# Kernel tuning notes

Hardware: AMD Instinct MI355X
Metric: run time of the kernel (lower is better)

Reference implementation:

```python
import jax, jax.numpy as jnp
import numpy as np

N_NODES, N_VARS, E = 100000, 50000, 640000
FEAT, H, L = 16, 128, 4
N_INT, K = 20000, 8  # integer vars with categorical heads, uniform domain size


def _mlp2(x, W1, b1, W2, b2):
    return jnp.maximum(x @ W1 + b1, 0.0) @ W2 + b2


def setup_inputs() -> dict:
    key = jax.random.key(0)
    ks = jax.random.split(key, 24)
    s = lambda i, shape, scale: jax.random.normal(ks[i], shape, dtype=jnp.float32) * scale
    inp = {
        "x": jax.random.normal(ks[0], (N_NODES, FEAT), dtype=jnp.float32),
        "edge_index": jax.random.randint(ks[1], (2, E), 0, N_NODES, dtype=jnp.int32).astype(jnp.int64),
        "num_vars": N_VARS,
        # NodeEmbedder (var / cons)
        "ve_W1": s(2, (FEAT, H), 0.25), "ve_b1": jnp.zeros((H,), jnp.float32),
        "ve_W2": s(3, (H, H), 0.09),   "ve_b2": jnp.zeros((H,), jnp.float32),
        "ce_W1": s(4, (FEAT, H), 0.25), "ce_b1": jnp.zeros((H,), jnp.float32),
        "ce_W2": s(5, (H, H), 0.09),   "ce_b2": jnp.zeros((H,), jnp.float32),
        # GCN backbone: stacked per-layer params
        "conv_W": s(6, (L, H, H), 0.09), "conv_b": jnp.zeros((L, H), jnp.float32),
        "ref_W1": s(7, (L, H, H), 0.09), "ref_b1": jnp.zeros((L, H), jnp.float32),
        "ref_W2": s(8, (L, H, H), 0.09), "ref_b2": jnp.zeros((L, H), jnp.float32),
        # Bernoulli head: H -> H//2 -> 1
        "bh_W1": s(9, (H, H // 2), 0.09), "bh_b1": jnp.zeros((H // 2,), jnp.float32),
        "bh_W2": s(10, (H // 2, 1), 0.12), "bh_b2": jnp.zeros((1,), jnp.float32),
        # Categorical heads: one Linear(H, K) per integer variable, batched
        "cat_W": s(11, (N_INT, H, K), 0.09),
        "cat_b": jnp.zeros((N_INT, K), jnp.float32),
    }
    return inp


def reference(x, edge_index, num_vars,
              ve_W1, ve_b1, ve_W2, ve_b2,
              ce_W1, ce_b1, ce_W2, ce_b2,
              conv_W, conv_b, ref_W1, ref_b1, ref_W2, ref_b2,
              bh_W1, bh_b1, bh_W2, bh_b2,
              cat_W, cat_b):
    N = x.shape[0]
    src, dst = edge_index[0], edge_index[1]
    # GCN normalization with self-loops: deg includes the self edge
    deg = jax.ops.segment_sum(jnp.ones((src.shape[0],), x.dtype), dst, num_segments=N) + 1.0
    dinv_sqrt = jax.lax.rsqrt(deg)
    enorm = dinv_sqrt[src] * dinv_sqrt[dst]      # [E]
    self_norm = (1.0 / deg)[:, None]             # [N,1] self-loop weight deg^-1

    var_h = _mlp2(x[:num_vars], ve_W1, ve_b1, ve_W2, ve_b2)
    cons_h = _mlp2(x[num_vars:], ce_W1, ce_b1, ce_W2, ce_b2)
    h = jnp.concatenate([var_h, cons_h], axis=0)  # [N,H]

    def gcn_conv(xin, W, b):
        hw = xin @ W
        agg = jax.ops.segment_sum(hw[src] * enorm[:, None], dst, num_segments=N)
        return agg + hw * self_norm + b

    def layer(xc, p):
        W, b, W1, b1, W2, b2 = p
        h_ = jnp.maximum(gcn_conv(xc, W, b), 0.0)
        return xc + _mlp2(h_, W1, b1, W2, b2), None

    h, _ = jax.lax.scan(layer, h, (conv_W, conv_b, ref_W1, ref_b1, ref_W2, ref_b2))

    vh = h[:num_vars]
    bern_logits = _mlp2(vh, bh_W1, bh_b1, bh_W2, bh_b2)[:, 0]          # [num_vars]
    n_int = cat_W.shape[0]
    cat_logits = jnp.einsum('nh,nhk->nk', vh[:n_int], cat_W) + cat_b    # [n_int,K]
    return bern_logits, cat_logits
```

## Files before the change

### kernel.cpp

```cpp
#include <hip/hip_runtime.h>
#include <hip/hip_bf16.h>

#define NN 100000
#define NV 50000
#define NE 640000
#define FEAT 16
#define HD 128
#define NL 4
#define NI 20000
#define KK 8
#define SCAN_BLK 98
#define LDP 136
#define WE_STRIDE (128*32 + 128*128)

typedef __hip_bfloat16 bf16;
typedef __attribute__((ext_vector_type(8))) short short8;
typedef __attribute__((ext_vector_type(4))) float f32x4;

static __device__ __forceinline__ ushort f2bu(float f) {
    __hip_bfloat16 b = __float2bfloat16(f);
    return *reinterpret_cast<ushort*>(&b);
}
static __device__ __forceinline__ float bu2f(ushort u) {
    __hip_bfloat16 b = *reinterpret_cast<__hip_bfloat16*>(&u);
    return __bfloat162float(b);
}

__global__ void k_deg_init(float* deg) {
    int i = blockIdx.x * blockDim.x + threadIdx.x;
    if (i < NN) deg[i] = 1.0f;
}

__global__ void k_deg_scatter(const int* __restrict__ ei, float* deg) {
    int e = blockIdx.x * blockDim.x + threadIdx.x;
    if (e < NE) atomicAdd(&deg[ei[NE + e]], 1.0f);
}

__global__ void k_deg_fin(const float* __restrict__ deg, float* dinv, float* selfn) {
    int i = blockIdx.x * blockDim.x + threadIdx.x;
    if (i < NN) {
        float d = deg[i];
        dinv[i]  = rsqrtf(d);
        selfn[i] = 1.0f / d;
    }
}

__global__ void k_scan_part(const float* __restrict__ deg, int* __restrict__ part) {
    __shared__ int s[256];
    const int t = threadIdx.x;
    const int i = blockIdx.x * 1024 + t * 4;
    int sum = 0;
#pragma unroll
    for (int j = 0; j < 4; ++j)
        if (i + j < NN) sum += (int)deg[i + j] - 1;
    s[t] = sum;
    __syncthreads();
    for (int off = 128; off > 0; off >>= 1) {
        if (t < off) s[t] += s[t + off];
        __syncthreads();
    }
    if (t == 0) part[blockIdx.x] = s[0];
}

__global__ void k_scan_mid(const int* __restrict__ part, int* __restrict__ blockoff,
                           int* __restrict__ row_ptr) {
    __shared__ int s[128];
    const int t = threadIdx.x;
    int v = (t < SCAN_BLK) ? part[t] : 0;
    s[t] = v;
    __syncthreads();
    for (int off = 1; off < 128; off <<= 1) {
        int u = (t >= off) ? s[t - off] : 0;
        __syncthreads();
        s[t] += u;
        __syncthreads();
    }
    if (t < SCAN_BLK) blockoff[t] = s[t] - v;
    if (t == 0) row_ptr[NN] = NE;
}

__global__ void k_scan_apply(const float* __restrict__ deg,
                             const int* __restrict__ blockoff,
                             int* __restrict__ row_ptr, int* __restrict__ cnt) {
    __shared__ int s[256];
    const int t = threadIdx.x;
    const int i = blockIdx.x * 1024 + t * 4;
    int c[4];
    int tsum = 0;
#pragma unroll
    for (int j = 0; j < 4; ++j) {
        c[j] = (i + j < NN) ? (int)deg[i + j] - 1 : 0;
        tsum += c[j];
    }
    s[t] = tsum;
    __syncthreads();
    for (int off = 1; off < 256; off <<= 1) {
        int u = (t >= off) ? s[t - off] : 0;
        __syncthreads();
        s[t] += u;
        __syncthreads();
    }
    int off = blockoff[blockIdx.x] + s[t] - tsum;
#pragma unroll
    for (int j = 0; j < 4; ++j) {
        if (i + j < NN) {
            row_ptr[i + j] = off;
            cnt[i + j] = 0;
            off += c[j];
        }
    }
}

__global__ void k_csr_fill(const int* __restrict__ ei,
                           const int* __restrict__ row_ptr, int* __restrict__ cnt,
                           const float* __restrict__ dinv,
                           int* __restrict__ col, float* __restrict__ wgt) {
    int e = blockIdx.x * blockDim.x + threadIdx.x;
    if (e >= NE) return;
    const int s = ei[e];
    const int d = ei[NE + e];
    const int pos = row_ptr[d] + atomicAdd(&cnt[d], 1);
    col[pos] = s;
    wgt[pos] = dinv[s] * dinv[d];
}

__global__ void k_wprep(const float* __restrict__ conv_W,
                        const float* __restrict__ ref_W1,
                        const float* __restrict__ ref_W2,
                        ushort* __restrict__ wt) {
    const int mat = blockIdx.x >> 7;
    const int j = blockIdx.x & 127;
    const int k = threadIdx.x;
    const float* src = (mat < 4) ? conv_W + (size_t)mat * HD * HD
                     : (mat < 8) ? ref_W1 + (size_t)(mat - 4) * HD * HD
                                 : ref_W2 + (size_t)(mat - 8) * HD * HD;
    wt[(size_t)mat * HD * HD + j * HD + k] = f2bu(src[k * HD + j]);
}

__global__ void k_wprep_embed(const float* __restrict__ vW1, const float* __restrict__ vW2,
                              const float* __restrict__ cW1, const float* __restrict__ cW2,
                              ushort* __restrict__ wte) {
    const int side = blockIdx.x >> 7;
    const int j = blockIdx.x & 127;
    const int k = threadIdx.x;
    const float* W1 = side ? cW1 : vW1;
    const float* W2 = side ? cW2 : vW2;
    ushort* o = wte + (size_t)side * WE_STRIDE;
    if (k < 32) o[j * 32 + k] = (k < FEAT) ? f2bu(W1[k * HD + j]) : (ushort)0;
    o[128 * 32 + j * HD + k] = f2bu(W2[k * HD + j]);
}

__global__ __launch_bounds__(256, 4) void k_embed_mfma(
        const float* __restrict__ x,
        const ushort* __restrict__ W1t, const float* __restrict__ b1,
        const ushort* __restrict__ W2t, const float* __restrict__ b2,
        int nbase, int nend,
        ushort* __restrict__ hb) {
    const int lane = threadIdx.x & 63, w = threadIdx.x >> 6;
    const int l15 = lane & 15, lg = lane >> 4;
    const int rowb = nbase + blockIdx.x * 128;
    __shared__ ushort hsm[128][LDP];

#pragma unroll
    for (int rt = 0; rt < 2; ++rt) {
        const int r = rowb + w * 32 + rt * 16 + l15;
        const int rc = r < nend ? r : nend - 1;
        short8 a = {0, 0, 0, 0, 0, 0, 0, 0};
        if (lg < 2) {
            const float* xp = x + (size_t)rc * FEAT + lg * 8;
#pragma unroll
            for (int i = 0; i < 8; ++i) a[i] = (short)f2bu(xp[i]);
        }
#pragma unroll
        for (int jt = 0; jt < 8; ++jt) {
            const float bv = b1[jt * 16 + l15];
            f32x4 acc = {bv, bv, bv, bv};
            short8 b = *reinterpret_cast<const short8*>(&W1t[(jt * 16 + l15) * 32 + lg * 8]);
            acc = __builtin_amdgcn_mfma_f32_16x16x32_bf16(a, b, acc, 0, 0, 0);
#pragma unroll
            for (int rr = 0; rr < 4; ++rr)
                hsm[w * 32 + rt * 16 + lg * 4 + rr][jt * 16 + l15] =
                    f2bu(fmaxf(acc[rr], 0.0f));
        }
    }
    __syncthreads();

#pragma unroll
    for (int rt = 0; rt < 2; ++rt) {
        f32x4 acc[8];
#pragma unroll
        for (int jt = 0; jt < 8; ++jt) {
            const float bv = b2[jt * 16 + l15];
            f32x4 v = {bv, bv, bv, bv};
            acc[jt] = v;
        }
#pragma unroll
        for (int ks = 0; ks < 4; ++ks) {
            short8 a = *reinterpret_cast<const short8*>(&hsm[w * 32 + rt * 16 + l15][ks * 32 + lg * 8]);
#pragma unroll
            for (int jt = 0; jt < 8; ++jt) {
                short8 b = *reinterpret_cast<const short8*>(&W2t[(jt * 16 + l15) * HD + ks * 32 + lg * 8]);
                acc[jt] = __builtin_amdgcn_mfma_f32_16x16x32_bf16(a, b, acc[jt], 0, 0, 0);
            }
        }
#pragma unroll
        for (int jt = 0; jt < 8; ++jt)
#pragma unroll
            for (int rr = 0; rr < 4; ++rr) {
                const int row = rowb + w * 32 + rt * 16 + lg * 4 + rr;
                if (row < nend)
                    hb[(size_t)row * HD + jt * 16 + l15] = f2bu(acc[jt][rr]);
            }
    }
}

__global__ __launch_bounds__(256) void k_hw(
                     const ushort* __restrict__ hb, const ushort* __restrict__ Wt,
                     ushort* __restrict__ hwb) {
    const int lane = threadIdx.x & 63;
    const int w = threadIdx.x >> 6;
    const int row0 = blockIdx.x * 128 + w * 32;
    const int l15 = lane & 15, lg = lane >> 4;

    const f32x4 zero = {0.f, 0.f, 0.f, 0.f};
    f32x4 acc[2][8];
#pragma unroll
    for (int rt = 0; rt < 2; ++rt)
#pragma unroll
        for (int jt = 0; jt < 8; ++jt) acc[rt][jt] = zero;

#pragma unroll
    for (int ks = 0; ks < 4; ++ks) {
        short8 a[2];
#pragma unroll
        for (int rt = 0; rt < 2; ++rt) {
            int r = row0 + rt * 16 + l15;
            r = r < NN ? r : NN - 1;
            a[rt] = *reinterpret_cast<const short8*>(&hb[(size_t)r * HD + ks * 32 + lg * 8]);
        }
#pragma unroll
        for (int jt = 0; jt < 8; ++jt) {
            short8 b = *reinterpret_cast<const short8*>(&Wt[(jt * 16 + l15) * HD + ks * 32 + lg * 8]);
            acc[0][jt] = __builtin_amdgcn_mfma_f32_16x16x32_bf16(a[0], b, acc[0][jt], 0, 0, 0);
            acc[1][jt] = __builtin_amdgcn_mfma_f32_16x16x32_bf16(a[1], b, acc[1][jt], 0, 0, 0);
        }
    }
#pragma unroll
    for (int rt = 0; rt < 2; ++rt)
#pragma unroll
        for (int jt = 0; jt < 8; ++jt)
#pragma unroll
            for (int r = 0; r < 4; ++r) {
                int row = row0 + rt * 16 + lg * 4 + r;
                if (row < NN) hwb[(size_t)row * HD + jt * 16 + l15] = f2bu(acc[rt][jt][r]);
            }
}

__global__ __launch_bounds__(512, 4) void k_combine(
                          const ushort* __restrict__ hwb,
                          const int* __restrict__ row_ptr,
                          const int* __restrict__ col,
                          const float* __restrict__ wgt,
                          const float* __restrict__ selfn,
                          const float* __restrict__ cb,
                          const ushort* __restrict__ Wt1, const float* __restrict__ b1,
                          const ushort* __restrict__ Wt2, const float* __restrict__ b2,
                          ushort* __restrict__ hb) {
    const int t = threadIdx.x;
    const int n0 = blockIdx.x * 64;
    __shared__ ushort hs[64][LDP];
    __shared__ ushort hid[64][LDP];
    __shared__ int rp[65];

    if (t <= 64) {
        int idx = n0 + t;
        rp[t] = row_ptr[idx < NN ? idx : NN];
    }
    __syncthreads();

    const int lane = t & 63, w = t >> 6;
    {
        const int c0 = 2 * lane;
        const float cbx = cb[c0], cby = cb[c0 + 1];
        float accx[8], accy[8];
        int ecur[8], eend[8];
        int rounds = 0;
#pragma unroll
        for (int m = 0; m < 8; ++m) {
            const int node = n0 + w * 8 + m;
            const int nc = node < NN ? node : NN - 1;
            const uint hv = *reinterpret_cast<const uint*>(&hwb[(size_t)nc * HD + c0]);
            const float sn = selfn[nc];
            accx[m] = bu2f((ushort)(hv & 0xffffu)) * sn + cbx;
            accy[m] = bu2f((ushort)(hv >> 16)) * sn + cby;
            ecur[m] = rp[w * 8 + m];
            eend[m] = rp[w * 8 + m + 1];
            rounds = max(rounds, eend[m] - ecur[m]);
        }
#pragma unroll 1
        for (int r = 0; r < rounds; r += 2) {
            uint va[8], vb[8];
            float wa[8], wb[8];
            int ca[8], cc[8];
#pragma unroll
            for (int m = 0; m < 8; ++m) {
                const int e0 = ecur[m];
                const int a0 = (e0 < eend[m]) ? e0 : 0;
                const int a1 = (e0 + 1 < eend[m]) ? e0 + 1 : 0;
                wa[m] = (e0 < eend[m]) ? wgt[a0] : 0.0f;
                wb[m] = (e0 + 1 < eend[m]) ? wgt[a1] : 0.0f;
                ca[m] = col[a0];
                cc[m] = col[a1];
            }
#pragma unroll
            for (int m = 0; m < 8; ++m) {
                va[m] = *reinterpret_cast<const uint*>(&hwb[(size_t)ca[m] * HD + c0]);
                vb[m] = *reinterpret_cast<const uint*>(&hwb[(size_t)cc[m] * HD + c0]);
            }
#pragma unroll
            for (int m = 0; m < 8; ++m) {
                accx[m] += wa[m] * bu2f((ushort)(va[m] & 0xffffu));
                accy[m] += wa[m] * bu2f((ushort)(va[m] >> 16));
                accx[m] += wb[m] * bu2f((ushort)(vb[m] & 0xffffu));
                accy[m] += wb[m] * bu2f((ushort)(vb[m] >> 16));
            }
#pragma unroll
            for (int m = 0; m < 8; ++m) ecur[m] += 2;
        }
#pragma unroll
        for (int m = 0; m < 8; ++m) {
            const uint px = (uint)f2bu(fmaxf(accx[m], 0.0f));
            const uint py = (uint)f2bu(fmaxf(accy[m], 0.0f));
            *reinterpret_cast<uint*>(&hs[w * 8 + m][c0]) = px | (py << 16);
        }
    }
    __syncthreads();

    const int l15 = lane & 15, lg = lane >> 4;
    const int rt = (w & 3) * 16;
    const int c0 = (w >> 2) * 64;

    f32x4 acc1[4];
#pragma unroll
    for (int jt = 0; jt < 4; ++jt) {
        float bv = b1[c0 + jt * 16 + l15];
        f32x4 v = {bv, bv, bv, bv};
        acc1[jt] = v;
    }
#pragma unroll
    for (int ks = 0; ks < 4; ++ks) {
        short8 a = *reinterpret_cast<const short8*>(&hs[rt + l15][ks * 32 + lg * 8]);
#pragma unroll
        for (int jt = 0; jt < 4; ++jt) {
            short8 b = *reinterpret_cast<const short8*>(&Wt1[(c0 + jt * 16 + l15) * HD + ks * 32 + lg * 8]);
            acc1[jt] = __builtin_amdgcn_mfma_f32_16x16x32_bf16(a, b, acc1[jt], 0, 0, 0);
        }
    }
#pragma unroll
    for (int jt = 0; jt < 4; ++jt)
#pragma unroll
        for (int r = 0; r < 4; ++r)
            hid[rt + lg * 4 + r][c0 + jt * 16 + l15] = f2bu(fmaxf(acc1[jt][r], 0.0f));
    __syncthreads();

    f32x4 acc2[4];
#pragma unroll
    for (int jt = 0; jt < 4; ++jt) {
        float bv = b2[c0 + jt * 16 + l15];
        f32x4 v = {bv, bv, bv, bv};
        acc2[jt] = v;
    }
#pragma unroll
    for (int ks = 0; ks < 4; ++ks) {
        short8 a = *reinterpret_cast<const short8*>(&hid[rt + l15][ks * 32 + lg * 8]);
#pragma unroll
        for (int jt = 0; jt < 4; ++jt) {
            short8 b = *reinterpret_cast<const short8*>(&Wt2[(c0 + jt * 16 + l15) * HD + ks * 32 + lg * 8]);
            acc2[jt] = __builtin_amdgcn_mfma_f32_16x16x32_bf16(a, b, acc2[jt], 0, 0, 0);
        }
    }
#pragma unroll
    for (int jt = 0; jt < 4; ++jt)
#pragma unroll
        for (int r = 0; r < 4; ++r) {
            const int row = n0 + rt + lg * 4 + r;
            if (row < NN) {
                const size_t idx = (size_t)row * HD + c0 + jt * 16 + l15;
                hb[idx] = f2bu(acc2[jt][r] + bu2f(hb[idx]));
            }
        }
}

__global__ void k_bern(const ushort* __restrict__ hb,
                       const float* __restrict__ W1, const float* __restrict__ b1,
                       const float* __restrict__ W2, const float* __restrict__ b2,
                       float* __restrict__ out) {
    const long long t = (long long)blockIdx.x * blockDim.x + threadIdx.x;
    const int n = (int)(t >> 6);
    const int lane = (int)(t & 63);
    if (n >= NV) return;
    const ushort* hn = hb + (size_t)n * HD;
    float acc = b1[lane];
#pragma unroll 8
    for (int k = 0; k < HD; ++k) acc += bu2f(hn[k]) * W1[k * 64 + lane];
    float p = fmaxf(acc, 0.0f) * W2[lane];
#pragma unroll
    for (int off = 32; off > 0; off >>= 1) p += __shfl_down(p, off);
    if (lane == 0) out[n] = p + b2[0];
}

__global__ void k_cat(const ushort* __restrict__ hb,
                      const float* __restrict__ cW, const float* __restrict__ cb,
                      float* __restrict__ out) {
    const long long t = (long long)blockIdx.x * blockDim.x + threadIdx.x;
    const int n = (int)(t >> 6);
    const int lane = (int)(t & 63);
    if (n >= NI) return;
    const ushort* hn = hb + (size_t)n * HD;
    float p[KK];
#pragma unroll
    for (int k = 0; k < KK; ++k) p[k] = 0.0f;
#pragma unroll
    for (int half = 0; half < 2; ++half) {
        const int hh = lane + 64 * half;
        const float vh = bu2f(hn[hh]);
        const float* wp = cW + ((size_t)n * HD + hh) * KK;
#pragma unroll
        for (int k = 0; k < KK; ++k) p[k] += vh * wp[k];
    }
#pragma unroll
    for (int k = 0; k < KK; ++k) {
#pragma unroll
        for (int off = 32; off > 0; off >>= 1) p[k] += __shfl_down(p[k], off);
    }
    if (lane == 0) {
#pragma unroll
        for (int k = 0; k < KK; ++k) out[NV + (size_t)n * KK + k] = p[k] + cb[(size_t)n * KK + k];
    }
}

extern "C" void kernel_launch(void* const* d_in, const int* in_sizes, int n_in,
                              void* d_out, int out_size, void* d_ws, size_t ws_size,
                              hipStream_t stream) {
    const float* x  = (const float*)d_in[0];
    const int*   ei = (const int*)d_in[1];
    const float* ve_W1 = (const float*)d_in[3];
    const float* ve_b1 = (const float*)d_in[4];
    const float* ve_W2 = (const float*)d_in[5];
    const float* ve_b2 = (const float*)d_in[6];
    const float* ce_W1 = (const float*)d_in[7];
    const float* ce_b1 = (const float*)d_in[8];
    const float* ce_W2 = (const float*)d_in[9];
    const float* ce_b2 = (const float*)d_in[10];
    const float* conv_W = (const float*)d_in[11];
    const float* conv_b = (const float*)d_in[12];
    const float* ref_W1 = (const float*)d_in[13];
    const float* ref_b1 = (const float*)d_in[14];
    const float* ref_W2 = (const float*)d_in[15];
    const float* ref_b2 = (const float*)d_in[16];
    const float* bh_W1 = (const float*)d_in[17];
    const float* bh_b1 = (const float*)d_in[18];
    const float* bh_W2 = (const float*)d_in[19];
    const float* bh_b2 = (const float*)d_in[20];
    const float* cat_W = (const float*)d_in[21];
    const float* cat_b = (const float*)d_in[22];
    float* out = (float*)d_out;

    const size_t need = (size_t)(3 * NN + (NN + 1) + NN + 2 * NE + 2 * SCAN_BLK) * 4
                      + (size_t)NN * HD * 2
                      + (size_t)NN * HD * 2
                      + (size_t)12 * HD * HD * 2
                      + (size_t)2 * WE_STRIDE * 2;
    if (ws_size < need) return;

    float* deg     = (float*)d_ws;
    float* dinv    = deg + NN;
    float* selfn   = dinv + NN;
    int*   row_ptr = (int*)(selfn + NN);
    int*   cnt     = row_ptr + (NN + 1);
    int*   col     = cnt + NN;
    float* wgt     = (float*)(col + NE);
    int*   part    = (int*)(wgt + NE);
    int*   blockoff= part + SCAN_BLK;
    ushort* hwb    = (ushort*)(blockoff + SCAN_BLK);
    ushort* hb     = hwb + (size_t)NN * HD;
    ushort* wt     = hb + (size_t)NN * HD;
    ushort* wte    = wt + (size_t)12 * HD * HD;

    k_deg_init<<<(NN + 255) / 256, 256, 0, stream>>>(deg);
    k_deg_scatter<<<(NE + 255) / 256, 256, 0, stream>>>(ei, deg);
    k_deg_fin<<<(NN + 255) / 256, 256, 0, stream>>>(deg, dinv, selfn);
    k_scan_part<<<SCAN_BLK, 256, 0, stream>>>(deg, part);
    k_scan_mid<<<1, 128, 0, stream>>>(part, blockoff, row_ptr);
    k_scan_apply<<<SCAN_BLK, 256, 0, stream>>>(deg, blockoff, row_ptr, cnt);
    k_csr_fill<<<(NE + 255) / 256, 256, 0, stream>>>(ei, row_ptr, cnt, dinv, col, wgt);
    k_wprep<<<12 * 128, 128, 0, stream>>>(conv_W, ref_W1, ref_W2, wt);
    k_wprep_embed<<<256, 128, 0, stream>>>(ve_W1, ve_W2, ce_W1, ce_W2, wte);

    k_embed_mfma<<<(NV + 127) / 128, 256, 0, stream>>>(
        x, wte, ve_b1, wte + 128 * 32, ve_b2, 0, NV, hb);
    k_embed_mfma<<<(NN - NV + 127) / 128, 256, 0, stream>>>(
        x, wte + WE_STRIDE, ce_b1, wte + WE_STRIDE + 128 * 32, ce_b2, NV, NN, hb);

    for (int l = 0; l < NL; ++l) {
        k_hw<<<(NN + 127) / 128, 256, 0, stream>>>(hb, wt + (size_t)l * HD * HD, hwb);
        k_combine<<<(NN + 63) / 64, 512, 0, stream>>>(hwb, row_ptr, col, wgt, selfn,
                                               conv_b + (size_t)l * HD,
                                               wt + (size_t)(4 + l) * HD * HD,
                                               ref_b1 + (size_t)l * HD,
                                               wt + (size_t)(8 + l) * HD * HD,
                                               ref_b2 + (size_t)l * HD,
                                               hb);
    }

    k_bern<<<(NV * 64) / 256, 256, 0, stream>>>(hb, bh_W1, bh_b1, bh_W2, bh_b2, out);
    k_cat<<<(NI * 64) / 256, 256, 0, stream>>>(hb, cat_W, cat_b, out);
}
```

Measured before the change: 769.4 us.

## Fuse layer-0 hw matmul into embed, shrink combine blocks, vectorize cat loads

The embed kernel now also multiplies the freshly computed embedding by the first conv weight and writes hw for layer 0, so the separate k_hw launch for layer 0 is skipped along with one re-read of h. The combine kernel moves from 64 nodes and 512 threads per block to 32 nodes and 256 threads, with more blocks resident per CU. The categorical head loads its weights with float4 vector loads. The workspace also reserves an extra hw buffer (hwbB) that nothing uses.

After: 1.197 ms. 1.56x slower.

```diff
diff --git a/kernel.cpp b/kernel.cpp
--- a/kernel.cpp
+++ b/kernel.cpp
@@ -1,5 +1,6 @@
 #include <hip/hip_runtime.h>
 #include <hip/hip_bf16.h>
+
 
 #define NN 100000
 #define NV 50000
@@ -9,6 +10,7 @@
 #define NL 4
 #define NI 20000
 #define KK 8
+#define NB 32
 #define SCAN_BLK 98
 #define LDP 136
 #define WE_STRIDE (128*32 + 128*128)
@@ -154,8 +156,9 @@
         const float* __restrict__ x,
         const ushort* __restrict__ W1t, const float* __restrict__ b1,
         const ushort* __restrict__ W2t, const float* __restrict__ b2,
+        const ushort* __restrict__ Wtc,
         int nbase, int nend,
-        ushort* __restrict__ hb) {
+        ushort* __restrict__ hb, ushort* __restrict__ hwb) {
     const int lane = threadIdx.x & 63, w = threadIdx.x >> 6;
     const int l15 = lane & 15, lg = lane >> 4;
     const int rowb = nbase + blockIdx.x * 128;
@@ -208,8 +211,30 @@
 #pragma unroll
             for (int rr = 0; rr < 4; ++rr) {
                 const int row = rowb + w * 32 + rt * 16 + lg * 4 + rr;
+                const ushort hv = f2bu(acc[jt][rr]);
+                if (row < nend) hb[(size_t)row * HD + jt * 16 + l15] = hv;
+                hsm[w * 32 + rt * 16 + lg * 4 + rr][jt * 16 + l15] = hv;
+            }
+        f32x4 acc3[8];
+        const f32x4 zero = {0.f, 0.f, 0.f, 0.f};
+#pragma unroll
+        for (int jt = 0; jt < 8; ++jt) acc3[jt] = zero;
+#pragma unroll
+        for (int ks = 0; ks < 4; ++ks) {
+            short8 a = *reinterpret_cast<const short8*>(&hsm[w * 32 + rt * 16 + l15][ks * 32 + lg * 8]);
+#pragma unroll
+            for (int jt = 0; jt < 8; ++jt) {
+                short8 b = *reinterpret_cast<const short8*>(&Wtc[(jt * 16 + l15) * HD + ks * 32 + lg * 8]);
+                acc3[jt] = __builtin_amdgcn_mfma_f32_16x16x32_bf16(a, b, acc3[jt], 0, 0, 0);
+            }
+        }
+#pragma unroll
+        for (int jt = 0; jt < 8; ++jt)
+#pragma unroll
+            for (int rr = 0; rr < 4; ++rr) {
+                const int row = rowb + w * 32 + rt * 16 + lg * 4 + rr;
                 if (row < nend)
-                    hb[(size_t)row * HD + jt * 16 + l15] = f2bu(acc[jt][rr]);
+                    hwb[(size_t)row * HD + jt * 16 + l15] = f2bu(acc3[jt][rr]);
             }
     }
 }
@@ -256,7 +281,7 @@
             }
 }
 
-__global__ __launch_bounds__(512, 4) void k_combine(
+__global__ __launch_bounds__(256, 8) void k_combine(
                           const ushort* __restrict__ hwb,
                           const int* __restrict__ row_ptr,
                           const int* __restrict__ col,
@@ -267,12 +292,12 @@
                           const ushort* __restrict__ Wt2, const float* __restrict__ b2,
                           ushort* __restrict__ hb) {
     const int t = threadIdx.x;
-    const int n0 = blockIdx.x * 64;
-    __shared__ ushort hs[64][LDP];
-    __shared__ ushort hid[64][LDP];
-    __shared__ int rp[65];
-
-    if (t <= 64) {
+    const int n0 = blockIdx.x * NB;
+    __shared__ ushort hs[NB][LDP];
+    __shared__ ushort hid[NB][LDP];
+    __shared__ int rp[NB + 1];
+
+    if (t <= NB) {
         int idx = n0 + t;
         rp[t] = row_ptr[idx < NN ? idx : NN];
     }
@@ -337,8 +362,8 @@
     __syncthreads();
 
     const int l15 = lane & 15, lg = lane >> 4;
-    const int rt = (w & 3) * 16;
-    const int c0 = (w >> 2) * 64;
+    const int rt = (w & 1) * 16;
+    const int c0 = (w >> 1) * 64;
 
     f32x4 acc1[4];
 #pragma unroll
@@ -425,8 +450,10 @@
         const int hh = lane + 64 * half;
         const float vh = bu2f(hn[hh]);
         const float* wp = cW + ((size_t)n * HD + hh) * KK;
-#pragma unroll
-        for (int k = 0; k < KK; ++k) p[k] += vh * wp[k];
+        const float4 w0 = *reinterpret_cast<const float4*>(wp);
+        const float4 w1 = *reinterpret_cast<const float4*>(wp + 4);
+        p[0] += vh * w0.x; p[1] += vh * w0.y; p[2] += vh * w0.z; p[3] += vh * w0.w;
+        p[4] += vh * w1.x; p[5] += vh * w1.y; p[6] += vh * w1.z; p[7] += vh * w1.w;
     }
 #pragma unroll
     for (int k = 0; k < KK; ++k) {
@@ -467,8 +494,7 @@
     float* out = (float*)d_out;
 
     const size_t need = (size_t)(3 * NN + (NN + 1) + NN + 2 * NE + 2 * SCAN_BLK) * 4
-                      + (size_t)NN * HD * 2
-                      + (size_t)NN * HD * 2
+                      + (size_t)3 * NN * HD * 2
                       + (size_t)12 * HD * HD * 2
                       + (size_t)2 * WE_STRIDE * 2;
     if (ws_size < need) return;
@@ -482,8 +508,9 @@
     float* wgt     = (float*)(col + NE);
     int*   part    = (int*)(wgt + NE);
     int*   blockoff= part + SCAN_BLK;
-    ushort* hwb    = (ushort*)(blockoff + SCAN_BLK);
-    ushort* hb     = hwb + (size_t)NN * HD;
+    ushort* hwbA   = (ushort*)(blockoff + SCAN_BLK);
+    ushort* hwbB   = hwbA + (size_t)NN * HD;
+    ushort* hb     = hwbB + (size_t)NN * HD;
     ushort* wt     = hb + (size_t)NN * HD;
     ushort* wte    = wt + (size_t)12 * HD * HD;
 
@@ -498,13 +525,14 @@
     k_wprep_embed<<<256, 128, 0, stream>>>(ve_W1, ve_W2, ce_W1, ce_W2, wte);
 
     k_embed_mfma<<<(NV + 127) / 128, 256, 0, stream>>>(
-        x, wte, ve_b1, wte + 128 * 32, ve_b2, 0, NV, hb);
+        x, wte, ve_b1, wte + 128 * 32, ve_b2, wt, 0, NV, hb, hwbA);
     k_embed_mfma<<<(NN - NV + 127) / 128, 256, 0, stream>>>(
-        x, wte + WE_STRIDE, ce_b1, wte + WE_STRIDE + 128 * 32, ce_b2, NV, NN, hb);
+        x, wte + WE_STRIDE, ce_b1, wte + WE_STRIDE + 128 * 32, ce_b2, wt, NV, NN, hb, hwbA);
 
     for (int l = 0; l < NL; ++l) {
-        k_hw<<<(NN + 127) / 128, 256, 0, stream>>>(hb, wt + (size_t)l * HD * HD, hwb);
-        k_combine<<<(NN + 63) / 64, 512, 0, stream>>>(hwb, row_ptr, col, wgt, selfn,
+        if (l > 0)
+            k_hw<<<(NN + 127) / 128, 256, 0, stream>>>(hb, wt + (size_t)l * HD * HD, hwbA);
+        k_combine<<<NN / NB, 256, 0, stream>>>(hwbA, row_ptr, col, wgt, selfn,
                                                conv_b + (size_t)l * HD,
                                                wt + (size_t)(4 + l) * HD * HD,
                                                ref_b1 + (size_t)l * HD,
```
